# Performance work log

Hardware: AMD Instinct MI355X
Metric: run time of the kernel (lower is better)

Reference implementation:

```python
import jax, jax.numpy as jnp
import numpy as np

N, DEG, FIN, FOUT, K = 50000, 16, 32, 64, 3
E = N * DEG


def setup_inputs() -> dict:
    key = jax.random.key(0)
    ks = jax.random.split(key, 10)
    rng = np.random.default_rng(0)
    # unique edges sorted row-major (src*N+dst), ring guarantees deg_in/out>0
    ring = np.arange(N, dtype=np.int64) * N + (np.arange(N, dtype=np.int64) + 1) % N
    cand = np.unique(rng.integers(0, N * N, size=3 * E, dtype=np.int64))
    cand = np.setdiff1d(cand, ring, assume_unique=True)[: E - N]
    codes = np.sort(np.concatenate([cand, ring]))
    assert codes.shape[0] == E
    edge_index = jnp.asarray(np.stack([codes // N, codes % N]).astype(np.int32))
    X = jax.random.normal(ks[0], (N, FIN), jnp.float32)
    edge_weight = jax.random.uniform(ks[1], (E,), jnp.float32, 0.5, 1.5)
    cin = FIN + FOUT
    xav = float(np.sqrt(6.0 / (cin + FOUT)))
    def w(k):
        return jax.random.uniform(k, (2, K, cin, FOUT), jnp.float32, -xav, xav)
    return {
        'X': X, 'edge_index': edge_index, 'edge_weight': edge_weight,
        'Wz': w(ks[2]), 'bz': jnp.zeros((FOUT,), jnp.float32),
        'Wr': w(ks[3]), 'br': jnp.zeros((FOUT,), jnp.float32),
        'Wh': w(ks[4]), 'bh': jnp.zeros((FOUT,), jnp.float32),
    }


def _dconv(X, src, dst, rev_src, rev_dst, norm_out, norm_in, W, b):
    n = X.shape[0]
    def prop(x, s, d, nrm):  # out[d] += nrm * x[s]
        return jax.ops.segment_sum(nrm[:, None] * x[s], d, num_segments=n)
    H = X @ W[0, 0] + X @ W[1, 0]
    if W.shape[1] > 1:
        Tx1o = prop(X, src, dst, norm_out)
        Tx1i = prop(X, rev_src, rev_dst, norm_in)
        H = H + Tx1o @ W[0, 1] + Tx1i @ W[1, 1]
        for k in range(2, W.shape[1]):
            Tx1o = 2.0 * prop(Tx1o, src, dst, norm_out) - X
            Tx1i = 2.0 * prop(Tx1i, rev_src, rev_dst, norm_in) - X
            H = H + Tx1o @ W[0, k] + Tx1i @ W[1, k]
    return H + b


def reference(X, edge_index, edge_weight, Wz, bz, Wr, br, Wh, bh):
    n = X.shape[0]
    src, dst = edge_index[0], edge_index[1]
    deg_out = jax.ops.segment_sum(edge_weight, src, num_segments=n)
    deg_in = jax.ops.segment_sum(edge_weight, dst, num_segments=n)
    # faithful to original: both norms indexed by row (source)
    norm_out = 1.0 / deg_out[src]
    norm_in = 1.0 / deg_in[src]
    # reverse edges in dense_to_sparse(adj.T) order: sorted by (dst, src)
    order = jnp.argsort(dst.astype(jnp.int64) * n + src.astype(jnp.int64))
    rev_src, rev_dst = dst[order], src[order]
    H = jnp.zeros((n, Wz.shape[-1]), X.dtype)
    dc = lambda inp, W, b: _dconv(inp, src, dst, rev_src, rev_dst, norm_out, norm_in, W, b)
    Z = jax.nn.sigmoid(dc(jnp.concatenate([X, H], axis=1), Wz, bz))
    R = jax.nn.sigmoid(dc(jnp.concatenate([X, H], axis=1), Wr, br))
    H_tilde = jnp.tanh(dc(jnp.concatenate([X, H * R], axis=1), Wh, bh))
    return Z * H + (1.0 - Z) * H_tilde
```

## Files before the change

kernel.cpp:

```cpp
#include <hip/hip_runtime.h>
#include <hip/hip_fp16.h>
#include <cmath>

#define NN 50000
#define NE 800000
#define PADF 96
#define NBIN 391
#define NBLK 391
#define FCAP 3072
#define DST_HI 42949
#define SRC_CUT 33648

__device__ __forceinline__ unsigned short f2h(float f) {
  __half h = __float2half_rn(f);
  return *reinterpret_cast<unsigned short*>(&h);
}

typedef _Float16 half4 __attribute__((ext_vector_type(4)));
typedef float f32x4 __attribute__((ext_vector_type(4)));

__global__ __launch_bounds__(256) void k_aux(const float* __restrict__ X, const int* __restrict__ src,
                                             const int* __restrict__ dst, const float* __restrict__ ew,
                                             int* __restrict__ H,
                                             int* __restrict__ rptr, float* __restrict__ dout,
                                             const float* __restrict__ Wz, const float* __restrict__ Wh,
                                             unsigned short* __restrict__ WT, unsigned short* __restrict__ Xh,
                                             int* __restrict__ s0g) {
  __shared__ int hh[NBIN];
  __shared__ int s0l;
  int bid = blockIdx.x;
  int t = threadIdx.x;
  if (bid >= 667) {
    int h = bid - 667;
    hh[t] = 0;
    if (t + 256 < NBIN) hh[t + 256] = 0;
    if (t == 0) s0l = 0;
    __syncthreads();
    int my = 0;
#pragma unroll
    for (int r = 0; r < 8; ++r) {
      int e = h * 2048 + r * 256 + t;
      if (e < NE) {
        int d = dst[e];
        atomicAdd(&hh[d >> 7], 1);
        my += (d < DST_HI) ? 1 : 0;
        my += (d == DST_HI && src[e] < SRC_CUT) ? 1 : 0;
      }
    }
    atomicAdd(&s0l, my);
    __syncthreads();
    H[t * NBLK + h] = hh[t];
    if (t + 256 < NBIN) H[(t + 256) * NBLK + h] = hh[t + 256];
    if (t == 0) atomicAdd(s0g, s0l);
  } else if (bid < 196) {
    int i = bid * 256 + t;
    if (i >= NN) return;
    int lo = 0, hi = NE;
    while (lo < hi) { int m = (lo + hi) >> 1; if (src[m] < i) lo = m + 1; else hi = m; }
    int lo2 = lo, hi2 = NE;
    while (lo2 < hi2) { int m = (lo2 + hi2) >> 1; if (src[m] < i + 1) lo2 = m + 1; else hi2 = m; }
    rptr[i] = lo;
    if (i == NN - 1) rptr[NN] = lo2;
    float a = 0.f;
    for (int p = lo; p < lo2; ++p) a += ew[p];
    dout[i] = a;
  } else if (bid < 276) {
    int idx = (bid - 196) * 256 + t;
    int kk = idx >> 7, f = idx & 127;
    int blk = kk >> 5, c = kk & 31;
    const float* W = (f < 64) ? Wz : Wh;
    int fl = f & 63;
    float v;
    if (blk == 0)      v = W[c * 64 + fl] + W[18432 + c * 64 + fl];
    else if (blk == 1) v = W[6144 + c * 64 + fl];
    else if (blk == 2) v = W[18432 + 6144 + c * 64 + fl];
    else if (blk == 3) v = W[2 * 6144 + c * 64 + fl];
    else               v = W[18432 + 2 * 6144 + c * 64 + fl];
    WT[f * 160 + kk] = f2h(v);
  } else {
    int tt = (bid - 276) * 256 + t;
    int base = tt * 16;
    if (base >= NN * 32) return;
#pragma unroll
    for (int q = 0; q < 2; ++q) {
      const float4 a = *(const float4*)&X[base + q * 8];
      const float4 b = *(const float4*)&X[base + q * 8 + 4];
      ushort4 o1 = make_ushort4(f2h(a.x), f2h(a.y), f2h(a.z), f2h(a.w));
      ushort4 o2 = make_ushort4(f2h(b.x), f2h(b.y), f2h(b.z), f2h(b.w));
      *(ushort4*)&Xh[base + q * 8] = o1;
      *(ushort4*)&Xh[base + q * 8 + 4] = o2;
    }
  }
}

__global__ __launch_bounds__(512) void k_scanrow(int* __restrict__ H, int* __restrict__ rowtot) {
  __shared__ int tmp[512];
  int row = blockIdx.x;
  int t = threadIdx.x;
  int v = (t < NBLK) ? H[row * NBLK + t] : 0;
  tmp[t] = v;
  __syncthreads();
  for (int off = 1; off < 512; off <<= 1) {
    int u = (t >= (unsigned)off) ? tmp[t - off] : 0;
    __syncthreads();
    tmp[t] += u;
    __syncthreads();
  }
  if (t < NBLK) H[row * NBLK + t] = tmp[t] - v;
  if (t == 511) rowtot[row] = tmp[511];
}

__global__ __launch_bounds__(512) void k_part(const int* __restrict__ src, const int* __restrict__ dst,
                                              const int* __restrict__ P, const int* __restrict__ rowtot,
                                              unsigned long long* __restrict__ cmp64) {
  __shared__ int loc[NBIN];
  __shared__ int rs[512];
  __shared__ int rbase[NBIN];
  int h = blockIdx.x;
  int t = threadIdx.x;
  int v = (t < NBIN) ? rowtot[t] : 0;
  rs[t] = v;
  if (t < NBIN) loc[t] = 0;
  __syncthreads();
  for (int off = 1; off < 512; off <<= 1) {
    int u = (t >= (unsigned)off) ? rs[t - off] : 0;
    __syncthreads();
    rs[t] += u;
    __syncthreads();
  }
  if (t < NBIN) rbase[t] = rs[t] - v;
  __syncthreads();
#pragma unroll
  for (int r = 0; r < 4; ++r) {
    int e = h * 2048 + r * 512 + t;
    if (e < NE) {
      int d = dst[e];
      int bin = d >> 7;
      int rk = atomicAdd(&loc[bin], 1);
      int pos = rbase[bin] + P[bin * NBLK + h] + rk;
      cmp64[pos] = ((unsigned long long)(d & 127) << 48) |
                   ((unsigned long long)src[e] << 24) | (unsigned long long)e;
    }
  }
}

__global__ __launch_bounds__(512) void k_fine(const int* __restrict__ rowtot, const float* __restrict__ ew,
                                              const unsigned long long* __restrict__ cmp64,
                                              int2* __restrict__ cmp, int* __restrict__ sp,
                                              float* __restrict__ din) {
  __shared__ unsigned long long a1[FCAP], a2[FCAP];
  __shared__ int fh[128], fcnt[128], fo[129];
  __shared__ int bs[2];
  int cb = blockIdx.x;
  int t = threadIdx.x;
  if (t < 64) {
    int s = 0;
    for (int i = t; i < cb; i += 64) s += rowtot[i];
    s += __shfl_xor(s, 32, 64); s += __shfl_xor(s, 16, 64); s += __shfl_xor(s, 8, 64);
    s += __shfl_xor(s, 4, 64);  s += __shfl_xor(s, 2, 64);  s += __shfl_xor(s, 1, 64);
    if (t == 0) { bs[0] = s; bs[1] = s + rowtot[cb]; }
  }
  if (t < 128) { fh[t] = 0; fcnt[t] = 0; }
  __syncthreads();
  int base = bs[0];
  int m = bs[1] - base;
  if (m > FCAP) m = FCAP;
  for (int i = t; i < m; i += 512) {
    unsigned long long it = cmp64[base + i];
    a1[i] = it;
    atomicAdd(&fh[(int)(it >> 48)], 1);
  }
  __syncthreads();
  if (t < 64) {
    int v0 = fh[t * 2], v1 = fh[t * 2 + 1];
    int pair = v0 + v1;
    int run = pair;
    for (int off = 1; off < 64; off <<= 1) {
      int v = __shfl_up(run, off, 64);
      if (t >= off) run += v;
    }
    int excl = run - pair;
    fo[t * 2] = excl; fo[t * 2 + 1] = excl + v0;
    if (t == 63) fo[128] = excl + pair;
  }
  __syncthreads();
  for (int i = t; i < m; i += 512) {
    unsigned long long it = a1[i];
    int b = (int)(it >> 48);
    int p2 = fo[b] + atomicAdd(&fcnt[b], 1);
    a2[p2] = it;
  }
  if (t < 128) {
    int d = cb * 128 + t;
    if (d <= NN) sp[d] = base + fo[t];
  }
  __syncthreads();
  for (int i = t; i < m; i += 512) {
    unsigned long long it = a2[i];
    int e = (int)(it & 0xFFFFFF);
    int sc = (int)((it >> 24) & 0xFFFF);
    int d = cb * 128 + (int)(it >> 48);
    cmp[base + i] = make_int2(e, (int)(((unsigned)d << 16) | (unsigned)sc));
  }
  int nd = t >> 2, ln = t & 3;
  int d = cb * 128 + nd;
  if (d < NN) {
    float s = 0.f;
    int e0 = fo[nd], e1 = fo[nd + 1];
    for (int i = e0 + ln; i < e1; i += 4) s += ew[(int)(a2[i] & 0xFFFFFF)];
    s += __shfl_down(s, 2, 4);
    s += __shfl_down(s, 1, 4);
    if (ln == 0) din[d] = s;
  }
}

__global__ __launch_bounds__(256) void k_sortw(const int* __restrict__ sp, const int2* __restrict__ cmp,
                                               const int* __restrict__ rawsrc,
                                               const float* __restrict__ dout, const float* __restrict__ din,
                                               const int* __restrict__ s0g,
                                               int2* __restrict__ cnf, int2* __restrict__ cnr) {
  int wv = (blockIdx.x * 256 + threadIdx.x) >> 6;
  int lane = threadIdx.x & 63;
  if (wv >= NN) return;
  int b0 = sp[wv], b1 = sp[wv + 1];
  int n = b1 - b0;
  int s0 = s0g[0];
  if (n > 64) {
    if (lane == 0) {
      int es[PADF]; unsigned ys[PADF];
      int nn = n > PADF ? PADF : n;
      for (int i = 0; i < nn; ++i) { int2 pe = cmp[b0 + i]; es[i] = pe.x; ys[i] = (unsigned)pe.y; }
      for (int i = 1; i < nn; ++i) {
        int ve = es[i]; unsigned vy = ys[i]; int j = i - 1;
        while (j >= 0 && ys[j] > vy) { es[j + 1] = es[j]; ys[j + 1] = ys[j]; --j; }
        es[j + 1] = ve; ys[j + 1] = vy;
      }
      for (int i = 0; i < nn; ++i) {
        int sc = (int)(ys[i] & 0xFFFF);
        cnf[b0 + i] = make_int2(sc, __float_as_int(1.0f / dout[sc]));
        int j = b0 + i - s0; if (j < 0) j += NE;
        cnr[es[i]] = make_int2(wv, __float_as_int(1.0f / din[rawsrc[j]]));
      }
    }
    return;
  }
  unsigned long long k = ~0ULL;
  if (lane < n) {
    int2 pe = cmp[b0 + lane];
    k = ((unsigned long long)(unsigned)pe.y << 32) | (unsigned)pe.x;
  }
  if (n > 1) {
#pragma unroll
    for (int kk = 2; kk <= 64; kk <<= 1) {
#pragma unroll
      for (int j = kk >> 1; j > 0; j >>= 1) {
        unsigned long long o = __shfl_xor(k, j, 64);
        bool lower = (lane & j) == 0;
        bool asc = (lane & kk) == 0;
        bool keepmin = (lower == asc);
        if (keepmin ? (o < k) : (o > k)) k = o;
      }
    }
  }
  if (lane < n) {
    int e = (int)(k & 0xffffffffu);
    int sc = (int)((k >> 32) & 0xFFFF);
    cnf[b0 + lane] = make_int2(sc, __float_as_int(1.0f / dout[sc]));
    int j = b0 + lane - s0; if (j < 0) j += NE;
    cnr[e] = make_int2(wv, __float_as_int(1.0f / din[rawsrc[j]]));
  }
}

__global__ __launch_bounds__(256) void k_prop2(const unsigned short* __restrict__ inA, const int* __restrict__ rpA,
                                               const int2* __restrict__ cnA, unsigned short* __restrict__ outAh,
                                               const unsigned short* __restrict__ inB, const int* __restrict__ rpB,
                                               const int2* __restrict__ cnB, unsigned short* __restrict__ outBh,
                                               const float* __restrict__ sub, float mul) {
  int t = blockIdx.x * 256 + threadIdx.x;
  const int half = NN * 8;
  const unsigned short* in; const int* rp; const int2* cn; unsigned short* outh;
  if (t < half) { in = inA; rp = rpA; cn = cnA; outh = outAh; }
  else          { in = inB; rp = rpB; cn = cnB; outh = outBh; t -= half; }
  int r = t >> 3;
  if (r >= NN) return;
  int lane8 = t & 7;
  int c4 = lane8 * 4;
  int b = rp[r], e2 = rp[r + 1];
  float a0[4] = {0.f, 0.f, 0.f, 0.f}, a1[4] = {0.f, 0.f, 0.f, 0.f};
  int p = b;
#define GATH(cc, ww) { \
    uint2 bv = *(const uint2*)&in[(cc) * 32 + c4]; \
    float2 f01 = __half22float2(*(const __half2*)&bv.x); \
    float2 f23 = __half22float2(*(const __half2*)&bv.y); \
    float* a = (jj & 1) ? a1 : a0; \
    a[0] += (ww) * f01.x; a[1] += (ww) * f01.y; \
    a[2] += (ww) * f23.x; a[3] += (ww) * f23.y; }
  for (; p + 16 <= e2; p += 16) {
    int2 u = cn[p + lane8];
    int2 v = cn[p + 8 + lane8];
#pragma unroll
    for (int jj = 0; jj < 8; ++jj) {
      int col = __shfl(u.x, jj, 8);
      float w = __int_as_float(__shfl(u.y, jj, 8));
      GATH(col, w)
    }
#pragma unroll
    for (int jj = 0; jj < 8; ++jj) {
      int col = __shfl(v.x, jj, 8);
      float w = __int_as_float(__shfl(v.y, jj, 8));
      GATH(col, w)
    }
  }
  for (; p + 8 <= e2; p += 8) {
    int2 u = cn[p + lane8];
#pragma unroll
    for (int jj = 0; jj < 8; ++jj) {
      int col = __shfl(u.x, jj, 8);
      float w = __int_as_float(__shfl(u.y, jj, 8));
      GATH(col, w)
    }
  }
  for (int jj = 0; p < e2; ++p) {
    int2 c1 = cn[p];
    float w = __int_as_float(c1.y);
    GATH(c1.x, w)
  }
#undef GATH
  float ax = a0[0] + a1[0], ay = a0[1] + a1[1], az = a0[2] + a1[2], aw = a0[3] + a1[3];
  float4 o;
  if (sub) {
    const float4 s = *(const float4*)&sub[r * 32 + c4];
    o.x = mul * ax - s.x; o.y = mul * ay - s.y; o.z = mul * az - s.z; o.w = mul * aw - s.w;
  } else {
    o.x = ax; o.y = ay; o.z = az; o.w = aw;
  }
  ushort4 oh = make_ushort4(f2h(o.x), f2h(o.y), f2h(o.z), f2h(o.w));
  *(ushort4*)&outh[r * 32 + c4] = oh;
}

__global__ __launch_bounds__(256) void k_gemm(const unsigned short* __restrict__ Xh,
                                              const unsigned short* __restrict__ T1oh,
                                              const unsigned short* __restrict__ T1ih,
                                              const unsigned short* __restrict__ T2oh,
                                              const unsigned short* __restrict__ T2ih,
                                              const unsigned short* __restrict__ WT,
                                              const float* __restrict__ bz, const float* __restrict__ bh,
                                              float* __restrict__ out) {
  __shared__ unsigned short wlds[128 * 168];
  const int tid = threadIdx.x;
  for (int i = tid; i < 128 * 20; i += 256) {
    int n = i / 20, o = i % 20;
    *(uint4*)&wlds[n * 168 + o * 8] = *(const uint4*)&WT[n * 160 + o * 8];
  }
  __syncthreads();
  const int l = tid & 63, wid = tid >> 6;
  const int m0 = wid * 16;
  const int rb = blockIdx.x * 64;
  int grow = rb + m0 + (l & 15); if (grow >= NN) grow = NN - 1;
  const int kg = (l >> 4) * 4;
  f32x4 acc[8];
#pragma unroll
  for (int t = 0; t < 8; ++t) acc[t] = (f32x4){0.f, 0.f, 0.f, 0.f};
  const unsigned short* srcs[5] = {Xh, T1oh, T1ih, T2oh, T2ih};
#pragma unroll
  for (int s = 0; s < 5; ++s) {
    const unsigned short* A = srcs[s];
#pragma unroll
    for (int h2 = 0; h2 < 2; ++h2) {
      const int kk = h2 * 16;
      half4 af = *(const half4*)&A[grow * 32 + kk + kg];
      const int kglob = s * 32 + kk + kg;
#pragma unroll
      for (int t = 0; t < 8; ++t) {
        half4 bf = *(const half4*)&wlds[(t * 16 + (l & 15)) * 168 + kglob];
        acc[t] = __builtin_amdgcn_mfma_f32_16x16x16f16(af, bf, acc[t], 0, 0, 0);
      }
    }
  }
  const int c = l & 15;
#pragma unroll
  for (int t = 0; t < 4; ++t) {
    int col = t * 16 + c;
    float bzv = bz[col], bhv = bh[col];
#pragma unroll
    for (int i = 0; i < 4; ++i) {
      int r = rb + m0 + (l >> 4) * 4 + i;
      if (r < NN) {
        float z = 1.f / (1.f + expf(-(acc[t][i] + bzv)));
        float hv = tanhf(acc[t + 4][i] + bhv);
        out[r * 64 + col] = (1.f - z) * hv;
      }
    }
  }
}

extern "C" void kernel_launch(void* const* d_in, const int* in_sizes, int n_in,
                              void* d_out, int out_size, void* d_ws, size_t ws_size,
                              hipStream_t stream) {
  const float* X  = (const float*)d_in[0];
  const int*   ei = (const int*)d_in[1];
  const float* ew = (const float*)d_in[2];
  const float* Wz = (const float*)d_in[3];
  const float* bz = (const float*)d_in[4];
  const float* Wh = (const float*)d_in[7];
  const float* bh = (const float*)d_in[8];
  float* out = (float*)d_out;
  const int* src = ei;
  const int* dst = ei + NE;

  char* p = (char*)d_ws;
  auto alloc = [&](size_t bytes) -> char* {
    char* r = p;
    p += (bytes + 255) & ~(size_t)255;
    return r;
  };
  unsigned short* Xh   = (unsigned short*)alloc((size_t)NN * 32 * 2);
  unsigned short* T1oh = (unsigned short*)alloc((size_t)NN * 32 * 2);
  unsigned short* T1ih = (unsigned short*)alloc((size_t)NN * 32 * 2);
  unsigned short* T2oh = (unsigned short*)alloc((size_t)NN * 32 * 2);
  unsigned short* T2ih = (unsigned short*)alloc((size_t)NN * 32 * 2);
  unsigned long long* cmp64 = (unsigned long long*)alloc((size_t)NE * 8);
  int2*  cmp     = (int2*)alloc((size_t)NE * 8);
  int2*  cnf     = (int2*)alloc((size_t)NE * 8);
  int2*  cnr     = (int2*)alloc((size_t)NE * 8);
  int*   H       = (int*)alloc((size_t)NBIN * NBLK * 4);
  int*   rowtot  = (int*)alloc(NBIN * 4);
  int*   sp      = (int*)alloc((NN + 1) * 4);
  int*   rptr    = (int*)alloc((NN + 1) * 4);
  float* dout    = (float*)alloc(NN * 4);
  float* din     = (float*)alloc(NN * 4);
  unsigned short* WT = (unsigned short*)alloc(128 * 160 * 2);
  int*   s0g     = (int*)alloc(256);

  hipMemsetAsync(s0g, 0, 4, stream);
  k_aux<<<1058, 256, 0, stream>>>(X, src, dst, ew, H, rptr, dout, Wz, Wh, WT, Xh, s0g);
  k_scanrow<<<NBIN, 512, 0, stream>>>(H, rowtot);
  k_part<<<NBLK, 512, 0, stream>>>(src, dst, H, rowtot, cmp64);
  k_fine<<<NBIN, 512, 0, stream>>>(rowtot, ew, cmp64, cmp, sp, din);
  k_sortw<<<12500, 256, 0, stream>>>(sp, cmp, src, dout, din, s0g, cnf, cnr);

  k_prop2<<<3125, 256, 0, stream>>>(Xh, sp, cnf, T1oh,
                                    Xh, rptr, cnr, T1ih, nullptr, 1.f);
  k_prop2<<<3125, 256, 0, stream>>>(T1oh, sp, cnf, T2oh,
                                    T1ih, rptr, cnr, T2ih, X, 2.f);

  k_gemm<<<782, 256, 0, stream>>>(Xh, T1oh, T1ih, T2oh, T2ih, WT, bz, bh, out);
}
```

Measured before the change: 233.5 us.

## Fuse per-row sort into k_fine via rank counting and defer reverse-weight lookup

Removes the k_sortw kernel and the cmp intermediate buffer. Rows are now ordered inside k_fine's shared-memory bins by counting each item's rank within its segment, and cnf/cnr are written directly from there. The reverse-edge weight 1/din[src] is no longer precomputed, because din is only finished later in k_fine. Instead cnr stores the raw source index and k_prop2 does the lookup and reciprocal on the fly. This trades a launch and a global round trip for O(deg^2) shared-memory rank work plus an extra dependent gather in each propagation pass.

New measurement: 225.4 us. 3.5% less time.

```diff
diff --git a/kernel.cpp b/kernel.cpp
--- a/kernel.cpp
+++ b/kernel.cpp
@@ -4,7 +4,6 @@
 
 #define NN 50000
 #define NE 800000
-#define PADF 96
 #define NBIN 391
 #define NBLK 391
 #define FCAP 3072
@@ -146,8 +145,10 @@
 
 __global__ __launch_bounds__(512) void k_fine(const int* __restrict__ rowtot, const float* __restrict__ ew,
                                               const unsigned long long* __restrict__ cmp64,
-                                              int2* __restrict__ cmp, int* __restrict__ sp,
-                                              float* __restrict__ din) {
+                                              const int* __restrict__ rawsrc, const float* __restrict__ dout,
+                                              const int* __restrict__ s0g,
+                                              int* __restrict__ sp, float* __restrict__ din,
+                                              int2* __restrict__ cnf, int2* __restrict__ cnr) {
   __shared__ unsigned long long a1[FCAP], a2[FCAP];
   __shared__ int fh[128], fcnt[128], fo[129];
   __shared__ int bs[2];
@@ -195,12 +196,19 @@
     if (d <= NN) sp[d] = base + fo[t];
   }
   __syncthreads();
+  const int s0 = s0g[0];
   for (int i = t; i < m; i += 512) {
     unsigned long long it = a2[i];
+    int seg = (int)(it >> 48);
+    int f0 = fo[seg], f1 = fo[seg + 1];
+    int rank = 0;
+    for (int q = f0; q < f1; ++q) rank += (a2[q] < it) ? 1 : 0;
     int e = (int)(it & 0xFFFFFF);
     int sc = (int)((it >> 24) & 0xFFFF);
-    int d = cb * 128 + (int)(it >> 48);
-    cmp[base + i] = make_int2(e, (int)(((unsigned)d << 16) | (unsigned)sc));
+    int d = cb * 128 + seg;
+    cnf[base + i] = make_int2(sc, __float_as_int(1.0f / dout[sc]));
+    int j = base + f0 + rank - s0; if (j < 0) j += NE;
+    cnr[e] = make_int2(d, rawsrc[j]);
   }
   int nd = t >> 2, ln = t & 3;
   int d = cb * 128 + nd;
@@ -214,73 +222,18 @@
   }
 }
 
-__global__ __launch_bounds__(256) void k_sortw(const int* __restrict__ sp, const int2* __restrict__ cmp,
-                                               const int* __restrict__ rawsrc,
-                                               const float* __restrict__ dout, const float* __restrict__ din,
-                                               const int* __restrict__ s0g,
-                                               int2* __restrict__ cnf, int2* __restrict__ cnr) {
-  int wv = (blockIdx.x * 256 + threadIdx.x) >> 6;
-  int lane = threadIdx.x & 63;
-  if (wv >= NN) return;
-  int b0 = sp[wv], b1 = sp[wv + 1];
-  int n = b1 - b0;
-  int s0 = s0g[0];
-  if (n > 64) {
-    if (lane == 0) {
-      int es[PADF]; unsigned ys[PADF];
-      int nn = n > PADF ? PADF : n;
-      for (int i = 0; i < nn; ++i) { int2 pe = cmp[b0 + i]; es[i] = pe.x; ys[i] = (unsigned)pe.y; }
-      for (int i = 1; i < nn; ++i) {
-        int ve = es[i]; unsigned vy = ys[i]; int j = i - 1;
-        while (j >= 0 && ys[j] > vy) { es[j + 1] = es[j]; ys[j + 1] = ys[j]; --j; }
-        es[j + 1] = ve; ys[j + 1] = vy;
-      }
-      for (int i = 0; i < nn; ++i) {
-        int sc = (int)(ys[i] & 0xFFFF);
-        cnf[b0 + i] = make_int2(sc, __float_as_int(1.0f / dout[sc]));
-        int j = b0 + i - s0; if (j < 0) j += NE;
-        cnr[es[i]] = make_int2(wv, __float_as_int(1.0f / din[rawsrc[j]]));
-      }
-    }
-    return;
-  }
-  unsigned long long k = ~0ULL;
-  if (lane < n) {
-    int2 pe = cmp[b0 + lane];
-    k = ((unsigned long long)(unsigned)pe.y << 32) | (unsigned)pe.x;
-  }
-  if (n > 1) {
-#pragma unroll
-    for (int kk = 2; kk <= 64; kk <<= 1) {
-#pragma unroll
-      for (int j = kk >> 1; j > 0; j >>= 1) {
-        unsigned long long o = __shfl_xor(k, j, 64);
-        bool lower = (lane & j) == 0;
-        bool asc = (lane & kk) == 0;
-        bool keepmin = (lower == asc);
-        if (keepmin ? (o < k) : (o > k)) k = o;
-      }
-    }
-  }
-  if (lane < n) {
-    int e = (int)(k & 0xffffffffu);
-    int sc = (int)((k >> 32) & 0xFFFF);
-    cnf[b0 + lane] = make_int2(sc, __float_as_int(1.0f / dout[sc]));
-    int j = b0 + lane - s0; if (j < 0) j += NE;
-    cnr[e] = make_int2(wv, __float_as_int(1.0f / din[rawsrc[j]]));
-  }
-}
-
 __global__ __launch_bounds__(256) void k_prop2(const unsigned short* __restrict__ inA, const int* __restrict__ rpA,
-                                               const int2* __restrict__ cnA, unsigned short* __restrict__ outAh,
+                                               const int2* __restrict__ cnA, const float* __restrict__ wiA,
+                                               unsigned short* __restrict__ outAh,
                                                const unsigned short* __restrict__ inB, const int* __restrict__ rpB,
-                                               const int2* __restrict__ cnB, unsigned short* __restrict__ outBh,
+                                               const int2* __restrict__ cnB, const float* __restrict__ wiB,
+                                               unsigned short* __restrict__ outBh,
                                                const float* __restrict__ sub, float mul) {
   int t = blockIdx.x * 256 + threadIdx.x;
   const int half = NN * 8;
-  const unsigned short* in; const int* rp; const int2* cn; unsigned short* outh;
-  if (t < half) { in = inA; rp = rpA; cn = cnA; outh = outAh; }
-  else          { in = inB; rp = rpB; cn = cnB; outh = outBh; t -= half; }
+  const unsigned short* in; const int* rp; const int2* cn; const float* wi; unsigned short* outh;
+  if (t < half) { in = inA; rp = rpA; cn = cnA; wi = wiA; outh = outAh; }
+  else          { in = inB; rp = rpB; cn = cnB; wi = wiB; outh = outBh; t -= half; }
   int r = t >> 3;
   if (r >= NN) return;
   int lane8 = t & 7;
@@ -298,31 +251,34 @@
   for (; p + 16 <= e2; p += 16) {
     int2 u = cn[p + lane8];
     int2 v = cn[p + 8 + lane8];
+    float uw = wi ? (1.0f / wi[u.y]) : __int_as_float(u.y);
+    float vw = wi ? (1.0f / wi[v.y]) : __int_as_float(v.y);
 #pragma unroll
     for (int jj = 0; jj < 8; ++jj) {
       int col = __shfl(u.x, jj, 8);
-      float w = __int_as_float(__shfl(u.y, jj, 8));
+      float w = __shfl(uw, jj, 8);
       GATH(col, w)
     }
 #pragma unroll
     for (int jj = 0; jj < 8; ++jj) {
       int col = __shfl(v.x, jj, 8);
-      float w = __int_as_float(__shfl(v.y, jj, 8));
+      float w = __shfl(vw, jj, 8);
       GATH(col, w)
     }
   }
   for (; p + 8 <= e2; p += 8) {
     int2 u = cn[p + lane8];
+    float uw = wi ? (1.0f / wi[u.y]) : __int_as_float(u.y);
 #pragma unroll
     for (int jj = 0; jj < 8; ++jj) {
       int col = __shfl(u.x, jj, 8);
-      float w = __int_as_float(__shfl(u.y, jj, 8));
+      float w = __shfl(uw, jj, 8);
       GATH(col, w)
     }
   }
   for (int jj = 0; p < e2; ++p) {
     int2 c1 = cn[p];
-    float w = __int_as_float(c1.y);
+    float w = wi ? (1.0f / wi[c1.y]) : __int_as_float(c1.y);
     GATH(c1.x, w)
   }
 #undef GATH
@@ -420,7 +376,6 @@
   unsigned short* T2oh = (unsigned short*)alloc((size_t)NN * 32 * 2);
   unsigned short* T2ih = (unsigned short*)alloc((size_t)NN * 32 * 2);
   unsigned long long* cmp64 = (unsigned long long*)alloc((size_t)NE * 8);
-  int2*  cmp     = (int2*)alloc((size_t)NE * 8);
   int2*  cnf     = (int2*)alloc((size_t)NE * 8);
   int2*  cnr     = (int2*)alloc((size_t)NE * 8);
   int*   H       = (int*)alloc((size_t)NBIN * NBLK * 4);
@@ -436,13 +391,12 @@
   k_aux<<<1058, 256, 0, stream>>>(X, src, dst, ew, H, rptr, dout, Wz, Wh, WT, Xh, s0g);
   k_scanrow<<<NBIN, 512, 0, stream>>>(H, rowtot);
   k_part<<<NBLK, 512, 0, stream>>>(src, dst, H, rowtot, cmp64);
-  k_fine<<<NBIN, 512, 0, stream>>>(rowtot, ew, cmp64, cmp, sp, din);
-  k_sortw<<<12500, 256, 0, stream>>>(sp, cmp, src, dout, din, s0g, cnf, cnr);
-
-  k_prop2<<<3125, 256, 0, stream>>>(Xh, sp, cnf, T1oh,
-                                    Xh, rptr, cnr, T1ih, nullptr, 1.f);
-  k_prop2<<<3125, 256, 0, stream>>>(T1oh, sp, cnf, T2oh,
-                                    T1ih, rptr, cnr, T2ih, X, 2.f);
+  k_fine<<<NBIN, 512, 0, stream>>>(rowtot, ew, cmp64, src, dout, s0g, sp, din, cnf, cnr);
+
+  k_prop2<<<3125, 256, 0, stream>>>(Xh, sp, cnf, nullptr, T1oh,
+                                    Xh, rptr, cnr, din, T1ih, nullptr, 1.f);
+  k_prop2<<<3125, 256, 0, stream>>>(T1oh, sp, cnf, nullptr, T2oh,
+                                    T1ih, rptr, cnr, din, T2ih, X, 2.f);
 
   k_gemm<<<782, 256, 0, stream>>>(Xh, T1oh, T1ih, T2oh, T2ih, WT, bz, bh, out);
 }
```
